# Optimization experiments

Measured on AMD Instinct MI355X. Metric: run time of the kernel, lower is better.

The kernel has to match this reference:

```python
import jax, jax.numpy as jnp
import numpy as np


def setup_inputs() -> dict:
    key = jax.random.key(0)
    N, C, E, S = 200000, 128, 3200000, 5000
    k0, k1, k2 = jax.random.split(key, 3)
    x = jax.random.normal(k0, (N, C), dtype=jnp.float32)
    edge_index = jax.random.randint(k1, (2, E), 0, N, dtype=jnp.int32)
    starts = (jnp.arange(S, dtype=jnp.int32) * (N // S))  # sorted sentence start offsets
    node1_indices = starts
    node2_indices = starts + 1
    sent_indices = starts + 2
    W = jax.random.normal(k2, (C, 1), dtype=jnp.float32) * 0.1
    b = jnp.zeros((1,), dtype=jnp.float32)
    return dict(x=x, edge_index=edge_index, node1_indices=node1_indices,
                node2_indices=node2_indices, sent_indices=sent_indices,
                W=W, b=b, alpha=4)


def _gcn_score(x, edge_index, W, b):
    # PyG GCNConv: h = xW; add self-loops; sym-normalized aggregation; + bias
    N = x.shape[0]
    h = x @ W  # [N, 1]
    row, col = edge_index[0], edge_index[1]
    ones = jnp.ones(row.shape[0], dtype=x.dtype)
    deg = jax.ops.segment_sum(ones, col, num_segments=N) + 1.0  # self-loop included
    dis = jax.lax.rsqrt(deg)
    norm = dis[row] * dis[col]
    agg = jax.ops.segment_sum(h[row] * norm[:, None], col, num_segments=N)
    out = agg + h * (dis * dis)[:, None]  # self-loop term, norm = 1/deg
    return (out + b).squeeze(-1)  # [N]


def reference(x, edge_index, node1_indices, node2_indices, sent_indices, W, b, alpha):
    N = x.shape[0]
    S = node1_indices.shape[0]
    score = _gcn_score(x, edge_index, W, b)  # [N]

    # per-sentence segment ids: segment i = [node1_indices[i], node1_indices[i+1])
    seg = jnp.searchsorted(node1_indices, jnp.arange(N, dtype=node1_indices.dtype), side='right') - 1
    seg = jnp.clip(seg, 0, S - 1)

    # numerically-stable per-segment softmax of scores
    m = jax.ops.segment_max(score, seg, num_segments=S)
    e = jnp.exp(score - m[seg])
    Z = jax.ops.segment_sum(e, seg, num_segments=S)
    p = e / Z[seg]  # normalized scores per sentence

    # cutoff = max(p) - alpha * std(p) per sentence (population std, as np.std)
    cnt = jax.ops.segment_sum(jnp.ones(N, dtype=p.dtype), seg, num_segments=S)
    pmax = jax.ops.segment_max(p, seg, num_segments=S)
    mean = jax.ops.segment_sum(p, seg, num_segments=S) / cnt
    var = jax.ops.segment_sum(p * p, seg, num_segments=S) / cnt - mean * mean
    std = jnp.sqrt(jnp.maximum(var, 0.0))
    cutoff = pmax - jnp.float32(alpha) * std
    keep = p >= cutoff[seg]

    # union with node1/node2/sent special nodes (always kept)
    keep = keep.at[node1_indices].set(True)
    keep = keep.at[node2_indices].set(True)
    keep = keep.at[sent_indices].set(True)

    # remap: position of each kept node in the compacted ordering
    pos = jnp.cumsum(keep.astype(jnp.int32)) - 1  # valid only where keep

    # gated node features (masked-dense form of x[perm] * tanh(score[perm]))
    x_out = jnp.where(keep[:, None], x * jnp.tanh(score)[:, None], 0.0)

    new_node1 = pos[node1_indices]
    new_node2 = pos[node2_indices]
    new_sent = pos[sent_indices]

    # filter_adj: keep edges with both endpoints kept, remap endpoints
    row, col = edge_index[0], edge_index[1]
    edge_keep = keep[row] & keep[col]
    new_edge_index = jnp.where(edge_keep[None, :], pos[edge_index], -1)

    return (x_out, new_edge_index, keep, edge_keep, new_node1, new_node2, new_sent)
```

## Files before the change

kernel.cpp:

```cpp
#include <hip/hip_runtime.h>
#include <math.h>

#define WAVE 64
#define FXSCALE 4398046511104.0
#define WINDOW 7936
#define NBMAX 32

typedef float vfloat4 __attribute__((ext_vector_type(4)));

__global__ void k_h(const float* __restrict__ x, const float* __restrict__ W,
                    double* __restrict__ h, int N, int C) {
    int t = blockIdx.x * blockDim.x + threadIdx.x;
    int row = t >> 5;
    int lane = t & 31;
    if (row >= N) return;
    const float4* xr = (const float4*)(x + (size_t)row * C);
    const float4* w4 = (const float4*)W;
    int C4 = C >> 2;
    double acc = 0.0;
    for (int c = lane; c < C4; c += 32) {
        float4 xv = xr[c];
        float4 wv = w4[c];
        acc += (double)xv.x * (double)wv.x + (double)xv.y * (double)wv.y
             + (double)xv.z * (double)wv.z + (double)xv.w * (double)wv.w;
    }
    #pragma unroll
    for (int o = 16; o > 0; o >>= 1) acc += __shfl_xor(acc, o);
    if (lane == 0) h[row] = acc;
}

__global__ void k_hist(const int* __restrict__ ecol, int* __restrict__ binCnt,
                       int E, int NB) {
    __shared__ int cnt[NBMAX];
    int tid = threadIdx.x;
    if (tid < NBMAX) cnt[tid] = 0;
    __syncthreads();
    for (long e = (long)blockIdx.x * blockDim.x + tid; e < E; e += (long)gridDim.x * blockDim.x)
        atomicAdd(&cnt[ecol[e] / WINDOW], 1);
    __syncthreads();
    if (tid < NB && cnt[tid] > 0) atomicAdd(&binCnt[tid], cnt[tid]);
}

__global__ void k_off(const int* __restrict__ binCnt, int* __restrict__ binOff,
                      int* __restrict__ binWr, int NB) {
    if (threadIdx.x != 0 || blockIdx.x != 0) return;
    int acc = 0;
    for (int i = 0; i < NB; i++) {
        binOff[i] = acc;
        binWr[i] = acc;
        acc += binCnt[i];
    }
    binOff[NB] = acc;
}

__global__ void k_bin(const int* __restrict__ erow, const int* __restrict__ ecol,
                      int* __restrict__ binWr, int* __restrict__ binnedRow,
                      unsigned short* __restrict__ binnedCol16, int E, int NB) {
    __shared__ int cnt[NBMAX];
    __shared__ int base[NBMAX];
    int tid = threadIdx.x;
    if (tid < NBMAX) cnt[tid] = 0;
    __syncthreads();
    long b0 = (long)blockIdx.x * 2048;
    int bArr[8], rArr[8], rowA[8], colA[8];
    #pragma unroll
    for (int k = 0; k < 8; k++) {
        long e = b0 + (long)k * 256 + tid;
        if (e < E) {
            int c = ecol[e];
            int b = c / WINDOW;
            bArr[k] = b; rowA[k] = erow[e]; colA[k] = c - b * WINDOW;
            rArr[k] = atomicAdd(&cnt[b], 1);
        } else bArr[k] = -1;
    }
    __syncthreads();
    if (tid < NB && cnt[tid] > 0) base[tid] = atomicAdd(&binWr[tid], cnt[tid]);
    __syncthreads();
    #pragma unroll
    for (int k = 0; k < 8; k++) {
        if (bArr[k] >= 0) {
            int idx = base[bArr[k]] + rArr[k];
            binnedRow[idx] = rowA[k];
            binnedCol16[idx] = (unsigned short)colA[k];
        }
    }
}

__global__ void k_degb(const unsigned short* __restrict__ binnedCol16,
                       const int* __restrict__ binOff,
                       unsigned int* __restrict__ partialDeg, int N, int Md) {
    __shared__ unsigned int cnt[WINDOW];
    int bin = blockIdx.x / Md, m = blockIdx.x % Md;
    int tid = threadIdx.x;
    for (int i = tid; i < WINDOW; i += blockDim.x) cnt[i] = 0;
    __syncthreads();
    int st = binOff[bin], en = binOff[bin + 1];
    for (int idx = st + m * (int)blockDim.x + tid; idx < en; idx += Md * (int)blockDim.x)
        atomicAdd(&cnt[binnedCol16[idx]], 1u);
    __syncthreads();
    int wb = bin * WINDOW;
    for (int i = tid; i < WINDOW && wb + i < N; i += blockDim.x)
        partialDeg[(size_t)m * N + wb + i] = cnt[i];
}

__global__ void k_dis_hd(const unsigned int* __restrict__ partialDeg,
                         const double* __restrict__ h,
                         double* __restrict__ dis, double* __restrict__ hd,
                         int N, int Md) {
    int i = blockIdx.x * blockDim.x + threadIdx.x;
    if (i >= N) return;
    unsigned int dsum = 0;
    for (int m = 0; m < Md; m++) dsum += partialDeg[(size_t)m * N + i];
    double d = 1.0 / sqrt((double)dsum + 1.0);
    dis[i] = d;
    hd[i] = h[i] * d;
}

__global__ void k_aggb(const int* __restrict__ binnedRow,
                       const unsigned short* __restrict__ binnedCol16,
                       const int* __restrict__ binOff,
                       const double* __restrict__ hd, const double* __restrict__ dis,
                       unsigned long long* __restrict__ partialAgg, int N, int Ma) {
    __shared__ unsigned long long acc[WINDOW];
    int bin = blockIdx.x / Ma, m = blockIdx.x % Ma;
    int tid = threadIdx.x;
    for (int i = tid; i < WINDOW; i += blockDim.x) acc[i] = 0ULL;
    __syncthreads();
    int st = binOff[bin], en = binOff[bin + 1];
    int wb = bin * WINDOW;
    for (int idx = st + m * (int)blockDim.x + tid; idx < en; idx += Ma * (int)blockDim.x) {
        int r = binnedRow[idx];
        int c16 = binnedCol16[idx];
        long long q = __double2ll_rn(hd[r] * dis[wb + c16] * FXSCALE);
        atomicAdd(&acc[c16], (unsigned long long)q);
    }
    __syncthreads();
    for (int i = tid; i < WINDOW && wb + i < N; i += blockDim.x)
        partialAgg[(size_t)m * N + wb + i] = acc[i];
}

__global__ void k_score(const unsigned long long* __restrict__ partialAgg,
                        const double* __restrict__ h, const double* __restrict__ dis,
                        const float* __restrict__ bptr,
                        float* __restrict__ score32, float* __restrict__ tg,
                        int N, int Ma) {
    int i = blockIdx.x * blockDim.x + threadIdx.x;
    if (i >= N) return;
    long long acc = 0;
    for (int m = 0; m < Ma; m++) acc += (long long)partialAgg[(size_t)m * N + i];
    double agg = (double)acc / FXSCALE;
    double d = dis[i];
    double sc = (agg + h[i] * (d * d)) + (double)bptr[0];
    score32[i] = (float)sc;
    tg[i] = (float)tanh(sc);
}

__global__ void k_seg_np(const float* __restrict__ score32, const int* __restrict__ starts,
                         float* __restrict__ p32, int* __restrict__ keepI,
                         const int* __restrict__ alphaPtr,
                         const int* __restrict__ n1, const int* __restrict__ n2,
                         const int* __restrict__ sent, int N, int S) {
    int g = blockIdx.x * blockDim.x + threadIdx.x;
    if (g >= S) return;
    int st = starts[g];
    int en = (g == S - 1) ? N : starts[g + 1];
    if (en <= st) return;

    int ai = alphaPtr[0];
    float alpha = (ai >= 0 && ai < 1000000) ? (float)ai : __int_as_float(ai);

    float m = -3.402823466e38f;
    for (int i = st; i < en; i++) m = fmaxf(m, score32[i]);

    float Z = 0.0f;
    for (int i = st; i < en; i++) {
        float dm = __fsub_rn(score32[i], m);
        float e = (float)exp((double)dm);
        p32[i] = e;
        Z = __fadd_rn(Z, e);
    }

    float sp = 0.0f, sq = 0.0f, pm = -3.402823466e38f;
    for (int i = st; i < en; i++) {
        float p = __fdiv_rn(p32[i], Z);
        p32[i] = p;
        sp = __fadd_rn(sp, p);
        sq = __fadd_rn(sq, __fmul_rn(p, p));
        pm = fmaxf(pm, p);
    }

    float cnt_ = (float)(en - st);
    float mean = __fdiv_rn(sp, cnt_);
    float var = __fsub_rn(__fdiv_rn(sq, cnt_), __fmul_rn(mean, mean));
    float sd = sqrtf(fmaxf(var, 0.0f));
    float cutoff = __fsub_rn(pm, __fmul_rn(alpha, sd));

    for (int i = st; i < en; i++) keepI[i] = (p32[i] >= cutoff) ? 1 : 0;

    keepI[n1[g]] = 1;
    keepI[n2[g]] = 1;
    keepI[sent[g]] = 1;
}

#define SCAN_CHUNK 2048

__global__ void k_scanA(const int* __restrict__ keepI, int* __restrict__ bs, int N) {
    int tid = threadIdx.x;
    long base = (long)blockIdx.x * SCAN_CHUNK + (long)tid * 8;
    int s = 0;
    #pragma unroll
    for (int k = 0; k < 8; k++) { long i = base + k; if (i < N) s += keepI[i]; }
    __shared__ int sm[256];
    sm[tid] = s; __syncthreads();
    for (int off = 128; off > 0; off >>= 1) {
        if (tid < off) sm[tid] += sm[tid + off];
        __syncthreads();
    }
    if (tid == 0) bs[blockIdx.x] = sm[0];
}

__global__ void k_scanB(const int* __restrict__ bs, int* __restrict__ bo, int nb) {
    __shared__ int sm[256];
    __shared__ int carrySh;
    int tid = threadIdx.x;
    if (tid == 0) carrySh = 0;
    __syncthreads();
    for (int base = 0; base < nb; base += 256) {
        int i = base + tid;
        int v = (i < nb) ? bs[i] : 0;
        sm[tid] = v; __syncthreads();
        for (int off = 1; off < 256; off <<= 1) {
            int t = (tid >= off) ? sm[tid - off] : 0;
            __syncthreads();
            sm[tid] += t;
            __syncthreads();
        }
        int incl = sm[tid];
        int total = sm[255];
        int carry = carrySh;
        if (i < nb) bo[i] = carry + incl - v;
        __syncthreads();
        if (tid == 0) carrySh = carry + total;
        __syncthreads();
    }
}

__global__ void k_scanC(const int* __restrict__ keepI, const int* __restrict__ bo,
                        const float* __restrict__ tg,
                        int* __restrict__ posTag, float* __restrict__ gate,
                        float* __restrict__ o_keep, int N) {
    int tid = threadIdx.x;
    long base = (long)blockIdx.x * SCAN_CHUNK + (long)tid * 8;
    int v[8];
    int th = 0;
    #pragma unroll
    for (int k = 0; k < 8; k++) {
        long i = base + k;
        v[k] = (i < N) ? keepI[i] : 0;
        th += v[k];
    }
    __shared__ int sm[256];
    sm[tid] = th; __syncthreads();
    for (int off = 1; off < 256; off <<= 1) {
        int t = (tid >= off) ? sm[tid - off] : 0;
        __syncthreads();
        sm[tid] += t;
        __syncthreads();
    }
    int excl = sm[tid] - th;
    int run = bo[blockIdx.x] + excl;
    #pragma unroll
    for (int k = 0; k < 8; k++) {
        long i = base + k;
        if (i < N) {
            posTag[i] = v[k] ? (run + v[k] - 1) : -1;
            gate[i] = v[k] ? tg[i] : 0.0f;
            o_keep[i] = v[k] ? 1.0f : 0.0f;
            run += v[k];
        }
    }
}

__global__ void k_out(const float4* __restrict__ x4, const float* __restrict__ gate,
                      float* __restrict__ o_x, long total4,
                      const int* __restrict__ erow, const int* __restrict__ ecol,
                      const int* __restrict__ posTag,
                      float* __restrict__ o_edge, float* __restrict__ o_ekeep, int E,
                      const int* __restrict__ n1, const int* __restrict__ n2,
                      const int* __restrict__ sent,
                      float* __restrict__ o_n1, float* __restrict__ o_n2,
                      float* __restrict__ o_sent, int S,
                      int nxb, int neb4) {
    int b = blockIdx.x;
    if (b < nxb) {
        long idx = (long)b * blockDim.x + threadIdx.x;
        if (idx >= total4) return;
        int row = (int)(idx >> 5);
        float g = gate[row];
        float4 v = x4[idx];
        vfloat4 r = { v.x * g, v.y * g, v.z * g, v.w * g };
        __builtin_nontemporal_store(r, (vfloat4*)o_x + idx);
    } else if (b < nxb + neb4) {
        long e0 = ((long)(b - nxb) * blockDim.x + threadIdx.x) * 4;
        if (e0 >= E) return;
        if (e0 + 3 < E) {
            int4 r4 = *(const int4*)(erow + e0);
            int4 c4 = *(const int4*)(ecol + e0);
            vfloat4 oer, oec, ok;
            #pragma unroll
            for (int k = 0; k < 4; k++) {
                int r = (&r4.x)[k], c = (&c4.x)[k];
                int pr = posTag[r], pc = posTag[c];
                bool ek = (pr >= 0) && (pc >= 0);
                oer[k] = ek ? (float)pr : -1.0f;
                oec[k] = ek ? (float)pc : -1.0f;
                ok[k]  = ek ? 1.0f : 0.0f;
            }
            __builtin_nontemporal_store(oer, (vfloat4*)(o_edge + e0));
            __builtin_nontemporal_store(oec, (vfloat4*)(o_edge + (size_t)E + e0));
            __builtin_nontemporal_store(ok,  (vfloat4*)(o_ekeep + e0));
        } else {
            for (long e = e0; e < E; e++) {
                int r = erow[e], c = ecol[e];
                int pr = posTag[r], pc = posTag[c];
                bool ek = (pr >= 0) && (pc >= 0);
                o_edge[e] = ek ? (float)pr : -1.0f;
                o_edge[(size_t)E + e] = ek ? (float)pc : -1.0f;
                o_ekeep[e] = ek ? 1.0f : 0.0f;
            }
        }
    } else {
        int i = (b - nxb - neb4) * blockDim.x + threadIdx.x;
        if (i >= S) return;
        o_n1[i] = (float)posTag[n1[i]];
        o_n2[i] = (float)posTag[n2[i]];
        o_sent[i] = (float)posTag[sent[i]];
    }
}

extern "C" void kernel_launch(void* const* d_in, const int* in_sizes, int n_in,
                              void* d_out, int out_size, void* d_ws, size_t ws_size,
                              hipStream_t stream) {
    const float* x    = (const float*)d_in[0];
    const int*   eidx = (const int*)d_in[1];
    const int*   n1   = (const int*)d_in[2];
    const int*   n2   = (const int*)d_in[3];
    const int*   sent = (const int*)d_in[4];
    const float* W    = (const float*)d_in[5];
    const float* bp   = (const float*)d_in[6];
    const int*   alphaPtr = (const int*)d_in[7];

    int C = in_sizes[5];
    int N = in_sizes[0] / C;
    int E = in_sizes[1] / 2;
    int S = in_sizes[2];

    const int* erow = eidx;
    const int* ecol = eidx + E;

    int NB = (N + WINDOW - 1) / WINDOW;
    const int Md = 8, Ma = 8;

    char* ws = (char*)d_ws;
    size_t off = 0;
    auto alloc = [&](size_t bytes) { void* p = ws + off; off += (bytes + 255) & ~(size_t)255; return p; };
    int*   binCnt = (int*)  alloc(NBMAX * 4);
    int*   binOff = (int*)  alloc((NBMAX + 1) * 4);
    int*   binWr  = (int*)  alloc(NBMAX * 4);
    int*   binnedRow = (int*)alloc((size_t)E * 4);
    unsigned short* binnedCol16 = (unsigned short*)alloc((size_t)E * 2);
    unsigned int* partialDeg = (unsigned int*)alloc((size_t)Md * N * 4);
    unsigned long long* partialAgg = (unsigned long long*)alloc((size_t)Ma * N * 8);
    double* h     = (double*)alloc((size_t)N * 8);
    double* dis   = (double*)alloc((size_t)N * 8);
    double* hd    = (double*)alloc((size_t)N * 8);
    float* score32 = (float*)alloc((size_t)N * 4);
    float* p32    = (float*)alloc((size_t)N * 4);
    float* tg     = (float*)alloc((size_t)N * 4);
    int*   keepI  = (int*)  alloc((size_t)N * 4);
    int*   posTag = (int*)  alloc((size_t)N * 4);
    float* gate   = (float*)alloc((size_t)N * 4);
    int nb = (N + SCAN_CHUNK - 1) / SCAN_CHUNK;
    int*   bs     = (int*)  alloc((size_t)nb * 4);
    int*   bo     = (int*)  alloc((size_t)nb * 4);

    float* o_x     = (float*)d_out;
    float* o_edge  = o_x + (size_t)N * C;
    float* o_keep  = o_edge + 2 * (size_t)E;
    float* o_ekeep = o_keep + N;
    float* o_n1    = o_ekeep + E;
    float* o_n2    = o_n1 + S;
    float* o_sent  = o_n2 + S;

    (void)hipMemsetAsync(binCnt, 0, NBMAX * 4, stream);

    k_h<<<(N * 32 + 255) / 256, 256, 0, stream>>>(x, W, h, N, C);
    k_hist<<<512, 256, 0, stream>>>(ecol, binCnt, E, NB);
    k_off<<<1, 64, 0, stream>>>(binCnt, binOff, binWr, NB);
    int nBatches = (int)(((long)E + 2047) / 2048);
    k_bin<<<nBatches, 256, 0, stream>>>(erow, ecol, binWr, binnedRow, binnedCol16, E, NB);
    k_degb<<<NB * Md, 256, 0, stream>>>(binnedCol16, binOff, partialDeg, N, Md);
    k_dis_hd<<<(N + 255) / 256, 256, 0, stream>>>(partialDeg, h, dis, hd, N, Md);
    k_aggb<<<NB * Ma, 256, 0, stream>>>(binnedRow, binnedCol16, binOff, hd, dis, partialAgg, N, Ma);
    k_score<<<(N + 255) / 256, 256, 0, stream>>>(partialAgg, h, dis, bp, score32, tg, N, Ma);
    k_seg_np<<<(S + 255) / 256, 256, 0, stream>>>(score32, n1, p32, keepI, alphaPtr, n1, n2, sent, N, S);
    k_scanA<<<nb, 256, 0, stream>>>(keepI, bs, N);
    k_scanB<<<1, 256, 0, stream>>>(bs, bo, nb);
    k_scanC<<<nb, 256, 0, stream>>>(keepI, bo, tg, posTag, gate, o_keep, N);

    long total4 = (long)N * (C / 4);
    int nxb = (int)((total4 + 255) / 256);
    long e4 = (E + 3) / 4;
    int neb4 = (int)((e4 + 255) / 256);
    int nsb = (S + 255) / 256;
    k_out<<<nxb + neb4 + nsb, 256, 0, stream>>>(
        (const float4*)x, gate, o_x, total4,
        erow, ecol, posTag, o_edge, o_ekeep, E,
        n1, n2, sent, o_n1, o_n2, o_sent, S, nxb, neb4);
}
```

Measured before the change: 265.1 us.

## Fuse h/hist kernels, stage binning through LDS, store positions as float

Merges the h dot-product kernel and the column histogram into one launch using block-index partitioning, which removes a launch and lets the two overlap. The binning kernel now loads edges with vectorized int4 reads, sorts each 2048-edge batch locally in shared memory by bin, then writes contiguous runs to global memory, turning scattered writes into coalesced ones at the cost of extra LDS traffic and a serial per-block prefix. The position array is stored as float so the output kernel skips int-to-float conversions.

```diff
diff --git a/kernel.cpp b/kernel.cpp
--- a/kernel.cpp
+++ b/kernel.cpp
@@ -5,40 +5,44 @@
 #define FXSCALE 4398046511104.0
 #define WINDOW 7936
 #define NBMAX 32
+#define BINB 2048
 
 typedef float vfloat4 __attribute__((ext_vector_type(4)));
 
-__global__ void k_h(const float* __restrict__ x, const float* __restrict__ W,
-                    double* __restrict__ h, int N, int C) {
-    int t = blockIdx.x * blockDim.x + threadIdx.x;
-    int row = t >> 5;
-    int lane = t & 31;
-    if (row >= N) return;
-    const float4* xr = (const float4*)(x + (size_t)row * C);
-    const float4* w4 = (const float4*)W;
-    int C4 = C >> 2;
-    double acc = 0.0;
-    for (int c = lane; c < C4; c += 32) {
-        float4 xv = xr[c];
-        float4 wv = w4[c];
-        acc += (double)xv.x * (double)wv.x + (double)xv.y * (double)wv.y
-             + (double)xv.z * (double)wv.z + (double)xv.w * (double)wv.w;
-    }
-    #pragma unroll
-    for (int o = 16; o > 0; o >>= 1) acc += __shfl_xor(acc, o);
-    if (lane == 0) h[row] = acc;
-}
-
-__global__ void k_hist(const int* __restrict__ ecol, int* __restrict__ binCnt,
-                       int E, int NB) {
-    __shared__ int cnt[NBMAX];
-    int tid = threadIdx.x;
-    if (tid < NBMAX) cnt[tid] = 0;
-    __syncthreads();
-    for (long e = (long)blockIdx.x * blockDim.x + tid; e < E; e += (long)gridDim.x * blockDim.x)
-        atomicAdd(&cnt[ecol[e] / WINDOW], 1);
-    __syncthreads();
-    if (tid < NB && cnt[tid] > 0) atomicAdd(&binCnt[tid], cnt[tid]);
+__global__ void k_h_hist(const float* __restrict__ x, const float* __restrict__ W,
+                         double* __restrict__ h,
+                         const int* __restrict__ ecol, int* __restrict__ binCnt,
+                         int N, int C, int E, int NB, int nhb) {
+    int b = blockIdx.x;
+    if (b < nhb) {
+        int t = b * 256 + threadIdx.x;
+        int row = t >> 5;
+        int lane = t & 31;
+        if (row >= N) return;
+        const float4* xr = (const float4*)(x + (size_t)row * C);
+        const float4* w4 = (const float4*)W;
+        int C4 = C >> 2;
+        double acc = 0.0;
+        for (int c = lane; c < C4; c += 32) {
+            float4 xv = xr[c];
+            float4 wv = w4[c];
+            acc += (double)xv.x * (double)wv.x + (double)xv.y * (double)wv.y
+                 + (double)xv.z * (double)wv.z + (double)xv.w * (double)wv.w;
+        }
+        #pragma unroll
+        for (int o = 16; o > 0; o >>= 1) acc += __shfl_xor(acc, o);
+        if (lane == 0) h[row] = acc;
+    } else {
+        __shared__ int cnt[NBMAX];
+        int tid = threadIdx.x;
+        if (tid < NBMAX) cnt[tid] = 0;
+        __syncthreads();
+        int hb = b - nhb;
+        for (long e = (long)hb * 256 + tid; e < E; e += 512L * 256)
+            atomicAdd(&cnt[ecol[e] / WINDOW], 1);
+        __syncthreads();
+        if (tid < NB && cnt[tid] > 0) atomicAdd(&binCnt[tid], cnt[tid]);
+    }
 }
 
 __global__ void k_off(const int* __restrict__ binCnt, int* __restrict__ binOff,
@@ -57,32 +61,69 @@
                       int* __restrict__ binWr, int* __restrict__ binnedRow,
                       unsigned short* __restrict__ binnedCol16, int E, int NB) {
     __shared__ int cnt[NBMAX];
-    __shared__ int base[NBMAX];
+    __shared__ int lbase[NBMAX];
+    __shared__ int gbase[NBMAX];
+    __shared__ int lrow[BINB];
+    __shared__ unsigned short lcol[BINB];
+    __shared__ unsigned char lbin[BINB];
     int tid = threadIdx.x;
     if (tid < NBMAX) cnt[tid] = 0;
     __syncthreads();
-    long b0 = (long)blockIdx.x * 2048;
-    int bArr[8], rArr[8], rowA[8], colA[8];
+    long b0 = (long)blockIdx.x * BINB;
+    int n = (int)((E - b0) < (long)BINB ? (E - b0) : (long)BINB);
+    int bA[8], rkA[8], rwA[8];
+    unsigned short clA[8];
+    #pragma unroll
+    for (int k = 0; k < 8; k++) bA[k] = -1;
+    int base_i = tid * 8;
+    if (base_i + 8 <= n) {
+        long e = b0 + base_i;
+        int4 r0 = *(const int4*)(erow + e), r1 = *(const int4*)(erow + e + 4);
+        int4 c0 = *(const int4*)(ecol + e), c1 = *(const int4*)(ecol + e + 4);
+        int rr[8] = {r0.x, r0.y, r0.z, r0.w, r1.x, r1.y, r1.z, r1.w};
+        int cc[8] = {c0.x, c0.y, c0.z, c0.w, c1.x, c1.y, c1.z, c1.w};
+        #pragma unroll
+        for (int k = 0; k < 8; k++) {
+            int c = cc[k];
+            int bb = c / WINDOW;
+            bA[k] = bb; rwA[k] = rr[k]; clA[k] = (unsigned short)(c - bb * WINDOW);
+            rkA[k] = atomicAdd(&cnt[bb], 1);
+        }
+    } else {
+        for (int k = 0; k < 8; k++) {
+            int i = base_i + k;
+            if (i < n) {
+                long e = b0 + i;
+                int c = ecol[e];
+                int bb = c / WINDOW;
+                bA[k] = bb; rwA[k] = erow[e]; clA[k] = (unsigned short)(c - bb * WINDOW);
+                rkA[k] = atomicAdd(&cnt[bb], 1);
+            }
+        }
+    }
+    __syncthreads();
+    if (tid == 0) {
+        int acc = 0;
+        for (int i = 0; i < NB; i++) { lbase[i] = acc; acc += cnt[i]; }
+    }
+    __syncthreads();
+    if (tid < NB && cnt[tid] > 0) gbase[tid] = atomicAdd(&binWr[tid], cnt[tid]);
+    __syncthreads();
     #pragma unroll
     for (int k = 0; k < 8; k++) {
-        long e = b0 + (long)k * 256 + tid;
-        if (e < E) {
-            int c = ecol[e];
-            int b = c / WINDOW;
-            bArr[k] = b; rowA[k] = erow[e]; colA[k] = c - b * WINDOW;
-            rArr[k] = atomicAdd(&cnt[b], 1);
-        } else bArr[k] = -1;
-    }
-    __syncthreads();
-    if (tid < NB && cnt[tid] > 0) base[tid] = atomicAdd(&binWr[tid], cnt[tid]);
-    __syncthreads();
-    #pragma unroll
-    for (int k = 0; k < 8; k++) {
-        if (bArr[k] >= 0) {
-            int idx = base[bArr[k]] + rArr[k];
-            binnedRow[idx] = rowA[k];
-            binnedCol16[idx] = (unsigned short)colA[k];
-        }
+        if (bA[k] >= 0) {
+            int l = lbase[bA[k]] + rkA[k];
+            lrow[l] = rwA[k];
+            lcol[l] = clA[k];
+            lbin[l] = (unsigned char)bA[k];
+        }
+    }
+    __syncthreads();
+    for (int l = tid; l < n; l += 256) {
+        int bb = lbin[l];
+        int g = gbase[bb] + (l - lbase[bb]);
+        binnedRow[g] = lrow[l];
+        binnedCol16[g] = lcol[l];
     }
 }
 
@@ -247,7 +288,7 @@
 
 __global__ void k_scanC(const int* __restrict__ keepI, const int* __restrict__ bo,
                         const float* __restrict__ tg,
-                        int* __restrict__ posTag, float* __restrict__ gate,
+                        float* __restrict__ posF, float* __restrict__ gate,
                         float* __restrict__ o_keep, int N) {
     int tid = threadIdx.x;
     long base = (long)blockIdx.x * SCAN_CHUNK + (long)tid * 8;
@@ -273,7 +314,7 @@
     for (int k = 0; k < 8; k++) {
         long i = base + k;
         if (i < N) {
-            posTag[i] = v[k] ? (run + v[k] - 1) : -1;
+            posF[i] = v[k] ? (float)(run + v[k] - 1) : -1.0f;
             gate[i] = v[k] ? tg[i] : 0.0f;
             o_keep[i] = v[k] ? 1.0f : 0.0f;
             run += v[k];
@@ -284,7 +325,7 @@
 __global__ void k_out(const float4* __restrict__ x4, const float* __restrict__ gate,
                       float* __restrict__ o_x, long total4,
                       const int* __restrict__ erow, const int* __restrict__ ecol,
-                      const int* __restrict__ posTag,
+                      const float* __restrict__ posF,
                       float* __restrict__ o_edge, float* __restrict__ o_ekeep, int E,
                       const int* __restrict__ n1, const int* __restrict__ n2,
                       const int* __restrict__ sent,
@@ -310,10 +351,10 @@
             #pragma unroll
             for (int k = 0; k < 4; k++) {
                 int r = (&r4.x)[k], c = (&c4.x)[k];
-                int pr = posTag[r], pc = posTag[c];
-                bool ek = (pr >= 0) && (pc >= 0);
-                oer[k] = ek ? (float)pr : -1.0f;
-                oec[k] = ek ? (float)pc : -1.0f;
+                float pr = posF[r], pc = posF[c];
+                bool ek = (pr >= 0.0f) && (pc >= 0.0f);
+                oer[k] = ek ? pr : -1.0f;
+                oec[k] = ek ? pc : -1.0f;
                 ok[k]  = ek ? 1.0f : 0.0f;
             }
             __builtin_nontemporal_store(oer, (vfloat4*)(o_edge + e0));
@@ -322,19 +363,19 @@
         } else {
             for (long e = e0; e < E; e++) {
                 int r = erow[e], c = ecol[e];
-                int pr = posTag[r], pc = posTag[c];
-                bool ek = (pr >= 0) && (pc >= 0);
-                o_edge[e] = ek ? (float)pr : -1.0f;
-                o_edge[(size_t)E + e] = ek ? (float)pc : -1.0f;
+                float pr = posF[r], pc = posF[c];
+                bool ek = (pr >= 0.0f) && (pc >= 0.0f);
+                o_edge[e] = ek ? pr : -1.0f;
+                o_edge[(size_t)E + e] = ek ? pc : -1.0f;
                 o_ekeep[e] = ek ? 1.0f : 0.0f;
             }
         }
     } else {
         int i = (b - nxb - neb4) * blockDim.x + threadIdx.x;
         if (i >= S) return;
-        o_n1[i] = (float)posTag[n1[i]];
-        o_n2[i] = (float)posTag[n2[i]];
-        o_sent[i] = (float)posTag[sent[i]];
+        o_n1[i] = posF[n1[i]];
+        o_n2[i] = posF[n2[i]];
+        o_sent[i] = posF[sent[i]];
     }
 }
 
@@ -378,7 +419,7 @@
     float* p32    = (float*)alloc((size_t)N * 4);
     float* tg     = (float*)alloc((size_t)N * 4);
     int*   keepI  = (int*)  alloc((size_t)N * 4);
-    int*   posTag = (int*)  alloc((size_t)N * 4);
+    float* posF   = (float*)alloc((size_t)N * 4);
     float* gate   = (float*)alloc((size_t)N * 4);
     int nb = (N + SCAN_CHUNK - 1) / SCAN_CHUNK;
     int*   bs     = (int*)  alloc((size_t)nb * 4);
@@ -394,10 +435,10 @@
 
     (void)hipMemsetAsync(binCnt, 0, NBMAX * 4, stream);
 
-    k_h<<<(N * 32 + 255) / 256, 256, 0, stream>>>(x, W, h, N, C);
-    k_hist<<<512, 256, 0, stream>>>(ecol, binCnt, E, NB);
+    int nhb = (N * 32 + 255) / 256;
+    k_h_hist<<<nhb + 512, 256, 0, stream>>>(x, W, h, ecol, binCnt, N, C, E, NB, nhb);
     k_off<<<1, 64, 0, stream>>>(binCnt, binOff, binWr, NB);
-    int nBatches = (int)(((long)E + 2047) / 2048);
+    int nBatches = (int)(((long)E + BINB - 1) / BINB);
     k_bin<<<nBatches, 256, 0, stream>>>(erow, ecol, binWr, binnedRow, binnedCol16, E, NB);
     k_degb<<<NB * Md, 256, 0, stream>>>(binnedCol16, binOff, partialDeg, N, Md);
     k_dis_hd<<<(N + 255) / 256, 256, 0, stream>>>(partialDeg, h, dis, hd, N, Md);
@@ -406,7 +447,7 @@
     k_seg_np<<<(S + 255) / 256, 256, 0, stream>>>(score32, n1, p32, keepI, alphaPtr, n1, n2, sent, N, S);
     k_scanA<<<nb, 256, 0, stream>>>(keepI, bs, N);
     k_scanB<<<1, 256, 0, stream>>>(bs, bo, nb);
-    k_scanC<<<nb, 256, 0, stream>>>(keepI, bo, tg, posTag, gate, o_keep, N);
+    k_scanC<<<nb, 256, 0, stream>>>(keepI, bo, tg, posF, gate, o_keep, N);
 
     long total4 = (long)N * (C / 4);
     int nxb = (int)((total4 + 255) / 256);
@@ -415,6 +456,6 @@
     int nsb = (S + 255) / 256;
     k_out<<<nxb + neb4 + nsb, 256, 0, stream>>>(
         (const float4*)x, gate, o_x, total4,
-        erow, ecol, posTag, o_edge, o_ekeep, E,
+        erow, ecol, posF, o_edge, o_ekeep, E,
         n1, n2, sent, o_n1, o_n2, o_sent, S, nxb, neb4);
 }
```

Measured after the change: 251.6 us. 1.05x faster.
